# Performance work log

Hardware: AMD Instinct MI355X
Metric: run time of the kernel (lower is better)

Reference implementation:

```python
import jax, jax.numpy as jnp
import numpy as np

B_, L_, D_, E_, N_, DR_, DC_ = 2, 2048, 1024, 2048, 16, 64, 4

def setup_inputs() -> dict:
    key = jax.random.key(0)
    ks = jax.random.split(key, 12)
    s = lambda fan: 1.0 / np.sqrt(fan)
    inp = {}
    inp['resid'] = jax.random.normal(ks[0], (B_, L_, D_), jnp.float32)
    inp['norm_w'] = jnp.ones((D_,), jnp.float32)
    inp['skip_w'] = jax.random.normal(ks[1], (E_, D_), jnp.float32) * s(D_)
    inp['in_w'] = jax.random.normal(ks[2], (E_, D_), jnp.float32) * s(D_)
    inp['conv_w'] = jax.random.normal(ks[3], (E_, DC_), jnp.float32) * s(DC_)
    inp['conv_b'] = jax.random.normal(ks[4], (E_,), jnp.float32) * 0.1
    inp['wd1'] = jax.random.normal(ks[5], (DR_, E_), jnp.float32) * s(E_)
    inp['wd2'] = jax.random.uniform(ks[6], (E_, DR_), jnp.float32, -1.0, 1.0) * (DR_ ** -0.5)
    # dt bias init: inverse softplus of dt in [dt_min, dt_max]
    dt = jnp.exp(jax.random.uniform(ks[7], (E_,), jnp.float32) * (np.log(0.1) - np.log(0.001)) + np.log(0.001))
    dt = jnp.clip(dt, 1e-4, None)
    inp['wd2_b'] = dt + jnp.log(-jnp.expm1(-dt))
    inp['wB'] = jax.random.normal(ks[8], (N_, E_), jnp.float32) * s(E_)
    inp['wC'] = jax.random.normal(ks[9], (N_, E_), jnp.float32) * s(E_)
    inp['A_log'] = jnp.log(jnp.broadcast_to(jnp.arange(1, N_ + 1, dtype=jnp.float32), (E_, N_)))
    inp['W_D'] = jnp.ones((E_,), jnp.float32)
    inp['out_w'] = jax.random.normal(ks[10], (D_, E_), jnp.float32) * s(E_)
    return inp


def reference(resid, norm_w, skip_w, in_w, conv_w, conv_b, wd1, wd2, wd2_b, wB, wC, A_log, W_D, out_w):
    eps = 1e-5
    # RMSNorm
    xn = resid * jax.lax.rsqrt(jnp.mean(resid * resid, axis=-1, keepdims=True) + eps) * norm_w
    skip = jnp.einsum('bld,ed->ble', xn, skip_w)          # [B,L,E]
    x = jnp.einsum('bld,ed->ble', xn, in_w)               # [B,L,E]
    # causal depthwise conv1d (padding d_conv-1, keep first L outputs)
    Dc = conv_w.shape[1]
    L = x.shape[1]
    xp = jnp.pad(x, ((0, 0), (Dc - 1, 0), (0, 0)))
    xc = conv_b + sum(xp[:, k:k + L, :] * conv_w[:, k] for k in range(Dc))
    x = jax.nn.silu(xc)                                   # ssm input [B,L,E]
    # input-dependent delta, B, C
    delta = jax.nn.softplus(jnp.einsum('blr,er->ble', jnp.einsum('ble,re->blr', x, wd1), wd2) + wd2_b)
    Bm = jnp.einsum('ble,ne->bln', x, wB)                 # [B,L,N]
    Cm = jnp.einsum('ble,ne->bln', x, wC)                 # [B,L,N]
    A = -jnp.exp(A_log)                                   # [E,N]
    # selective scan over L
    def step(h, inp):
        xt, dt, bt, ct = inp                              # [B,E],[B,E],[B,N],[B,N]
        h = jnp.exp(dt[:, :, None] * A) * h + (dt * xt)[:, :, None] * bt[:, None, :]
        y = jnp.einsum('ben,bn->be', h, ct)
        return h, y
    h0 = jnp.zeros((x.shape[0], A.shape[0], A.shape[1]), x.dtype)
    xs = (jnp.swapaxes(x, 0, 1), jnp.swapaxes(delta, 0, 1),
          jnp.swapaxes(Bm, 0, 1), jnp.swapaxes(Cm, 0, 1))
    _, ys = jax.lax.scan(step, h0, xs)                    # ys: [L,B,E]
    y = jnp.swapaxes(ys, 0, 1) + W_D * x                  # skip connection D*x
    y = y * jax.nn.silu(skip)                             # gate
    out = jnp.einsum('ble,de->bld', y, out_w)
    return resid + out
```

## Files before the change

### kernel.cpp

```cpp
#include <hip/hip_runtime.h>
#include <hip/hip_bf16.h>

#define B_ 2
#define L_ 2048
#define D_ 1024
#define E_ 2048
#define N_ 16
#define DR_ 64
#define DC_ 4
#define M_ (B_*L_)
#define SSEG 16
#define LSEG (L_/SSEG)
#define KS_ 8
#define CH 32
#define LOG2E 1.4426950408889634f

typedef __attribute__((ext_vector_type(8))) short bf16x8;
typedef __attribute__((ext_vector_type(4))) float f32x4;

__device__ __forceinline__ ushort f2bf(float x){
    union { float f; unsigned u; } v; v.f = x;
    unsigned r = v.u + 0x7FFFu + ((v.u >> 16) & 1u);
    return (ushort)(r >> 16);
}
__device__ __forceinline__ float bf2f(ushort u){
    union { unsigned u; float f; } v; v.u = ((unsigned)u) << 16;
    return v.f;
}
__device__ __forceinline__ float fexp2(float x){
    float r;
    asm("v_exp_f32 %0, %1" : "=v"(r) : "v"(x));
    return r;
}
__device__ __forceinline__ float fast_silu(float x){
    return x * __builtin_amdgcn_rcpf(1.f + __expf(-x));
}
__device__ __forceinline__ float softplus_f(float z){
    return (z > 20.f) ? z : __logf(1.f + __expf(z));
}

#define DPP_F(x, CTRL) __int_as_float(__builtin_amdgcn_update_dpp(0, __float_as_int(x), (CTRL), 0xf, 0xf, true))

__device__ __forceinline__ void gld16(const void* g, void* l){
    __builtin_amdgcn_global_load_lds(
        (const __attribute__((address_space(1))) unsigned int*)g,
        (__attribute__((address_space(3))) unsigned int*)l,
        16, 0, 0);
}

#define PR0 (E_*D_/4)
#define PR1 (2*PR0)
#define PR2 (3*PR0)
#define PR3 (PR2 + E_*DR_/4)
#define PR4 (PR3 + DR_*E_/4)
#define PR5 (PR4 + N_*E_/4)
#define PR6 (PR5 + N_*E_/4)
#define PR7 (PR6 + 32*E_/4)
#define PR8 (PR7 + 4*E_/4)
__global__ __launch_bounds__(256) void prep_k(const float* __restrict__ in_w,
                                              const float* __restrict__ skip_w,
                                              const float* __restrict__ out_w,
                                              const float* __restrict__ wd2,
                                              const float* __restrict__ wd1,
                                              const float* __restrict__ wB,
                                              const float* __restrict__ wC,
                                              const float* __restrict__ conv_w,
                                              ushort* __restrict__ wis,
                                              ushort* __restrict__ wo,
                                              ushort* __restrict__ wd2b,
                                              ushort* __restrict__ W96,
                                              float* __restrict__ cwT){
    int i = blockIdx.x * 256 + threadIdx.x;
    const float* src; ushort* dst; int off;
    if (i < PR0)      { src = in_w;   dst = wis;                       off = i; }
    else if (i < PR1) { src = skip_w; dst = wis + (size_t)E_*D_;       off = i - PR0; }
    else if (i < PR2) { src = out_w;  dst = wo;                        off = i - PR1; }
    else if (i < PR3) { src = wd2;    dst = wd2b;                      off = i - PR2; }
    else if (i < PR4) { src = wd1;    dst = W96;                       off = i - PR3; }
    else if (i < PR5) { src = wB;     dst = W96 + (size_t)64*E_;       off = i - PR4; }
    else if (i < PR6) { src = wC;     dst = W96 + (size_t)80*E_;       off = i - PR5; }
    else if (i < PR7) {
        ushort4 z = {0,0,0,0};
        ((ushort4*)(W96 + (size_t)96*E_))[i - PR6] = z;
        return;
    } else if (i < PR8) {
        int u = i - PR7;
        int k = u >> 9;
        int g = u & 511;
        float4 o;
        o.x = conv_w[(g*4 + 0)*4 + k];
        o.y = conv_w[(g*4 + 1)*4 + k];
        o.z = conv_w[(g*4 + 2)*4 + k];
        o.w = conv_w[(g*4 + 3)*4 + k];
        ((float4*)(cwT + (size_t)k * E_))[g] = o;
        return;
    } else return;
    float4 v = ((const float4*)src)[off];
    ushort4 o;
    o.x = f2bf(v.x); o.y = f2bf(v.y); o.z = f2bf(v.z); o.w = f2bf(v.w);
    ((ushort4*)dst)[off] = o;
}

__global__ __launch_bounds__(256) void rmsnorm_k(const float* __restrict__ resid,
                                                 const float* __restrict__ norm_w,
                                                 ushort* __restrict__ xn){
    int row = blockIdx.x;
    const float4* r = (const float4*)(resid + (size_t)row * D_);
    float4 v = r[threadIdx.x];
    float ss = v.x*v.x + v.y*v.y + v.z*v.z + v.w*v.w;
    for (int m = 32; m; m >>= 1) ss += __shfl_xor(ss, m);
    __shared__ float sred[4];
    if ((threadIdx.x & 63) == 0) sred[threadIdx.x >> 6] = ss;
    __syncthreads();
    float tot = sred[0] + sred[1] + sred[2] + sred[3];
    float scale = rsqrtf(tot / (float)D_ + 1e-5f);
    const float4* wv = (const float4*)norm_w;
    float4 w = wv[threadIdx.x];
    ushort4 o;
    o.x = f2bf(v.x * scale * w.x);
    o.y = f2bf(v.y * scale * w.y);
    o.z = f2bf(v.z * scale * w.z);
    o.w = f2bf(v.w * scale * w.w);
    ((ushort4*)(xn + (size_t)row * D_))[threadIdx.x] = o;
}

#define BM 128
#define BN 128
#define BK 64

__global__ __launch_bounds__(256)
void gemm_dual_k(const ushort* __restrict__ A, const ushort* __restrict__ Bm,
                 ushort* __restrict__ P1, ushort* __restrict__ P2){
    __shared__ __align__(16) ushort As[BM * BK];
    __shared__ __align__(16) ushort Bs[BN * BK];
    const int wid9 = (blockIdx.x & 7) * 128 + (blockIdx.x >> 3);
    const int col0 = (wid9 & 31) * BN;
    const int row0 = (wid9 >> 5) * BM;
    const int tid = threadIdx.x;
    const int lane = tid & 63;
    const int wid = tid >> 6;
    const int wm = wid >> 1, wn = wid & 1;
    f32x4 acc[4][4] = {};
    const int l8 = lane >> 3;
    const int cs = ((lane & 7) ^ (l8 & 7)) * 8;

    for (int k0 = 0; k0 < D_; k0 += BK){
        #pragma unroll
        for (int i = 0; i < 4; ++i){
            const int R0 = wid * 32 + i * 8;
            gld16(A + (size_t)(row0 + R0 + l8) * D_ + k0 + cs, As + R0 * BK);
            gld16(Bm + (size_t)(col0 + R0 + l8) * D_ + k0 + cs, Bs + R0 * BK);
        }
        __syncthreads();
        #pragma unroll
        for (int kk = 0; kk < 2; ++kk){
            bf16x8 af[4], bfr[4];
            const int krow = lane & 15;
            const int kcol = ((kk * 4 + (lane >> 4)) ^ (krow & 7)) * 8;
            #pragma unroll
            for (int mi = 0; mi < 4; ++mi)
                af[mi] = *(const bf16x8*)(As + (wm*64 + mi*16 + krow) * BK + kcol);
            #pragma unroll
            for (int ni = 0; ni < 4; ++ni)
                bfr[ni] = *(const bf16x8*)(Bs + (wn*64 + ni*16 + krow) * BK + kcol);
            #pragma unroll
            for (int mi = 0; mi < 4; ++mi)
                #pragma unroll
                for (int ni = 0; ni < 4; ++ni)
                    acc[mi][ni] = __builtin_amdgcn_mfma_f32_16x16x32_bf16(af[mi], bfr[ni], acc[mi][ni], 0, 0, 0);
        }
        __syncthreads();
    }
    ushort* base = (col0 < E_) ? P1 : P2;
    const int cb = (col0 < E_) ? col0 : col0 - E_;
    #pragma unroll
    for (int mi = 0; mi < 4; ++mi)
        #pragma unroll
        for (int ni = 0; ni < 4; ++ni)
            #pragma unroll
            for (int j = 0; j < 4; ++j){
                int r = row0 + wm*64 + mi*16 + (lane >> 4) * 4 + j;
                int c = cb + wn*64 + ni*16 + (lane & 15);
                base[(size_t)r * E_ + c] = f2bf(acc[mi][ni][j]);
            }
}

#define OBM 64
__global__ __launch_bounds__(256)
void gemm_out_k(const ushort* __restrict__ A, const ushort* __restrict__ Bm,
                float* __restrict__ Cp, const float* __restrict__ aux){
    __shared__ __align__(16) ushort As[OBM * BK];
    __shared__ __align__(16) ushort Bs[BN * BK];
    const int wid9 = (blockIdx.x & 7) * 64 + (blockIdx.x >> 3);
    const int col0 = (wid9 & 7) * BN;
    const int row0 = (wid9 >> 3) * OBM;
    const int tid = threadIdx.x;
    const int lane = tid & 63;
    const int wid = tid >> 6;
    const int wm = wid >> 1, wn = wid & 1;
    f32x4 acc[2][4] = {};
    const int l8 = lane >> 3;
    const int cs = ((lane & 7) ^ (l8 & 7)) * 8;

    for (int k0 = 0; k0 < E_; k0 += BK){
        #pragma unroll
        for (int i = 0; i < 2; ++i){
            const int R0 = wid * 16 + i * 8;
            gld16(A + (size_t)(row0 + R0 + l8) * E_ + k0 + cs, As + R0 * BK);
        }
        #pragma unroll
        for (int i = 0; i < 4; ++i){
            const int R0 = wid * 32 + i * 8;
            gld16(Bm + (size_t)(col0 + R0 + l8) * E_ + k0 + cs, Bs + R0 * BK);
        }
        __syncthreads();
        #pragma unroll
        for (int kk = 0; kk < 2; ++kk){
            bf16x8 af[2], bfr[4];
            const int krow = lane & 15;
            const int kcol = ((kk * 4 + (lane >> 4)) ^ (krow & 7)) * 8;
            #pragma unroll
            for (int mi = 0; mi < 2; ++mi)
                af[mi] = *(const bf16x8*)(As + (wm*32 + mi*16 + krow) * BK + kcol);
            #pragma unroll
            for (int ni = 0; ni < 4; ++ni)
                bfr[ni] = *(const bf16x8*)(Bs + (wn*64 + ni*16 + krow) * BK + kcol);
            #pragma unroll
            for (int mi = 0; mi < 2; ++mi)
                #pragma unroll
                for (int ni = 0; ni < 4; ++ni)
                    acc[mi][ni] = __builtin_amdgcn_mfma_f32_16x16x32_bf16(af[mi], bfr[ni], acc[mi][ni], 0, 0, 0);
        }
        __syncthreads();
    }
    #pragma unroll
    for (int mi = 0; mi < 2; ++mi)
        #pragma unroll
        for (int ni = 0; ni < 4; ++ni)
            #pragma unroll
            for (int j = 0; j < 4; ++j){
                int r = row0 + wm*32 + mi*16 + (lane >> 4) * 4 + j;
                int c = col0 + wn*64 + ni*16 + (lane & 15);
                size_t idx = (size_t)r * D_ + c;
                Cp[idx] = acc[mi][ni][j] + aux[idx];
            }
}

#define CBM 64
__global__ __launch_bounds__(256)
void gemm_c96_sk(const ushort* __restrict__ A, const ushort* __restrict__ Bm,
                 float* __restrict__ part){
    __shared__ __align__(16) ushort As[CBM * BK];
    __shared__ __align__(16) ushort Bs[128 * BK];
    const int ks = blockIdx.x;
    const int row0 = blockIdx.y * CBM;
    const int tid = threadIdx.x;
    const int lane = tid & 63;
    const int wid = tid >> 6;
    const int wm = wid >> 1, wn = wid & 1;
    f32x4 acc[2][4] = {};
    const int l8 = lane >> 3;
    const int cs = ((lane & 7) ^ (l8 & 7)) * 8;

    for (int k0 = ks * (E_ / KS_); k0 < (ks + 1) * (E_ / KS_); k0 += BK){
        #pragma unroll
        for (int i = 0; i < 2; ++i){
            const int R0 = wid * 16 + i * 8;
            gld16(A + (size_t)(row0 + R0 + l8) * E_ + k0 + cs, As + R0 * BK);
        }
        #pragma unroll
        for (int i = 0; i < 4; ++i){
            const int R0 = wid * 32 + i * 8;
            gld16(Bm + (size_t)(R0 + l8) * E_ + k0 + cs, Bs + R0 * BK);
        }
        __syncthreads();
        #pragma unroll
        for (int kk = 0; kk < 2; ++kk){
            bf16x8 af[2], bfr[4];
            const int krow = lane & 15;
            const int kcol = ((kk * 4 + (lane >> 4)) ^ (krow & 7)) * 8;
            #pragma unroll
            for (int mi = 0; mi < 2; ++mi)
                af[mi] = *(const bf16x8*)(As + (wm*32 + mi*16 + krow) * BK + kcol);
            #pragma unroll
            for (int ni = 0; ni < 4; ++ni)
                bfr[ni] = *(const bf16x8*)(Bs + (wn*64 + ni*16 + krow) * BK + kcol);
            #pragma unroll
            for (int mi = 0; mi < 2; ++mi)
                #pragma unroll
                for (int ni = 0; ni < 4; ++ni)
                    acc[mi][ni] = __builtin_amdgcn_mfma_f32_16x16x32_bf16(af[mi], bfr[ni], acc[mi][ni], 0, 0, 0);
        }
        __syncthreads();
    }
    float* dst = part + (size_t)ks * M_ * 128;
    #pragma unroll
    for (int mi = 0; mi < 2; ++mi)
        #pragma unroll
        for (int ni = 0; ni < 4; ++ni)
            #pragma unroll
            for (int j = 0; j < 4; ++j){
                int r = row0 + wm*32 + mi*16 + (lane >> 4) * 4 + j;
                int c = wn*64 + ni*16 + (lane & 15);
                dst[(size_t)r * 128 + c] = acc[mi][ni][j];
            }
}

__global__ __launch_bounds__(256) void c96_reduce_k(const float* __restrict__ part,
                                                    ushort* __restrict__ C96){
    int i4 = blockIdx.x * 256 + threadIdx.x;
    float4 a = *(const float4*)(part + (size_t)i4 * 4);
    #pragma unroll
    for (int k = 1; k < KS_; ++k){
        float4 b = *(const float4*)(part + (size_t)k * M_ * 128 + (size_t)i4 * 4);
        a.x += b.x; a.y += b.y; a.z += b.z; a.w += b.w;
    }
    ushort4 o;
    o.x = f2bf(a.x); o.y = f2bf(a.y); o.z = f2bf(a.z); o.w = f2bf(a.w);
    *(ushort4*)(C96 + (size_t)i4 * 4) = o;
}

__global__ __launch_bounds__(256) void conv_silu_k(const ushort* __restrict__ xpre,
                                                   const float* __restrict__ cwT,
                                                   const float* __restrict__ conv_b,
                                                   ushort* __restrict__ xb){
    int i4 = blockIdx.x * 256 + threadIdx.x;
    if (i4 >= M_ * E_ / 4) return;
    int idx = i4 * 4;
    int e = idx & (E_ - 1);
    int bl = idx >> 11;
    int t = bl & (L_ - 1);
    float4 b4 = *(const float4*)(conv_b + e);
    float a0 = b4.x, a1 = b4.y, a2 = b4.z, a3 = b4.w;
    #pragma unroll
    for (int k = 0; k < 4; ++k){
        int dt = 3 - k;
        if (t >= dt){
            ushort4 xv = *(const ushort4*)(xpre + idx - dt * E_);
            float4 wv = *(const float4*)(cwT + (size_t)k * E_ + e);
            a0 += bf2f(xv.x) * wv.x;
            a1 += bf2f(xv.y) * wv.y;
            a2 += bf2f(xv.z) * wv.z;
            a3 += bf2f(xv.w) * wv.w;
        }
    }
    ushort4 sb;
    sb.x = f2bf(fast_silu(a0));
    sb.y = f2bf(fast_silu(a1));
    sb.z = f2bf(fast_silu(a2));
    sb.w = f2bf(fast_silu(a3));
    *(ushort4*)(xb + idx) = sb;
}

#define SF2 36
#define SYD 20

__device__ __forceinline__ void seg_swz(int& b, int& s, int& e0){
    int lin = blockIdx.x + 128 * (blockIdx.y + 16 * blockIdx.z);
    int swz = (lin & 7) * 512 + (lin >> 3);
    e0 = (swz & 127) * 16;
    s  = (swz >> 7) & 15;
    b  = swz >> 11;
}

__global__ __launch_bounds__(256, 8) void seg1_k(const ushort* __restrict__ xb,
                                              const ushort* __restrict__ C96,
                                              const ushort* __restrict__ wd2b,
                                              const float* __restrict__ wd2_bias,
                                              const float* __restrict__ A_log,
                                              float* __restrict__ F,
                                              float* __restrict__ segdt){
    int b, s, e0; seg_swz(b, s, e0);
    const int tid = threadIdx.x;
    const int lane = tid & 63, wid = tid >> 6;
    const int n = tid & 15, ei = tid >> 4;
    const int e = e0 + ei;
    const float Aen2 = -__expf(A_log[e * N_ + n]) * LOG2E;
    float h = 0.f;
    __shared__ __align__(16) ushort sxr[CH][72];
    __shared__ __align__(16) ushort swd2[16][72];
    __shared__ __align__(16) ushort sxu[16][40];
    __shared__ float sd[16][SF2], sdx[16][SF2], sB[16][SF2];
    __shared__ float ssdt[2][16];
    const int tq = tid >> 3, qc = tid & 7;

    if (tid < 128){
        int r = tid >> 3, cc = (tid & 7) * 8;
        *(uint4*)&swd2[r][cc] = *(const uint4*)(wd2b + (size_t)(e0 + r) * DR_ + cc);
    }
    const float bias = wd2_bias[e0 + (lane & 15)];
    float psdt = 0.f;

    for (int c = 0; c < LSEG / CH; ++c){
        int t0 = s * LSEG + c * CH;
        size_t row = (size_t)(b * L_ + t0 + tq);
        *(uint4*)&sxr[tq][qc * 8] = *(const uint4*)(C96 + row * 128 + qc * 8);
        ushort2 rB = *(const ushort2*)(C96 + row * 128 + 64 + qc * 2);
        ushort2 xu = *(const ushort2*)(xb + row * E_ + e0 + qc * 2);
        sB[qc*2+0][tq] = bf2f(rB.x); sB[qc*2+1][tq] = bf2f(rB.y);
        sxu[qc*2+0][tq] = xu.x; sxu[qc*2+1][tq] = xu.y;
        __syncthreads();
        if (wid < 2){
            f32x4 dacc = {};
            #pragma unroll
            for (int kk = 0; kk < 2; ++kk){
                bf16x8 af = *(const bf16x8*)&sxr[wid*16 + (lane & 15)][kk*32 + (lane >> 4)*8];
                bf16x8 bf = *(const bf16x8*)&swd2[lane & 15][kk*32 + (lane >> 4)*8];
                dacc = __builtin_amdgcn_mfma_f32_16x16x32_bf16(af, bf, dacc, 0, 0, 0);
            }
            const int crow = lane & 15;
            const int ttc = wid*16 + (lane >> 4)*4;
            float4 dv;
            dv.x = softplus_f(dacc[0] + bias);
            dv.y = softplus_f(dacc[1] + bias);
            dv.z = softplus_f(dacc[2] + bias);
            dv.w = softplus_f(dacc[3] + bias);
            *(float4*)&sd[crow][ttc] = dv;
            psdt += dv.x + dv.y + dv.z + dv.w;
            ushort4 xu4 = *(const ushort4*)&sxu[crow][ttc];
            float4 dxv;
            dxv.x = dv.x * bf2f(xu4.x); dxv.y = dv.y * bf2f(xu4.y);
            dxv.z = dv.z * bf2f(xu4.z); dxv.w = dv.w * bf2f(xu4.w);
            *(float4*)&sdx[crow][ttc] = dxv;
        }
        __syncthreads();
        #pragma unroll
        for (int t = 0; t < CH; t += 4){
            float4 d4  = *(const float4*)&sd[ei][t];
            float4 dx4 = *(const float4*)&sdx[ei][t];
            float4 b4  = *(const float4*)&sB[n][t];
            h = fexp2(d4.x*Aen2)*h + dx4.x*b4.x;
            h = fexp2(d4.y*Aen2)*h + dx4.y*b4.y;
            h = fexp2(d4.z*Aen2)*h + dx4.z*b4.z;
            h = fexp2(d4.w*Aen2)*h + dx4.w*b4.w;
        }
        __syncthreads();
    }
    if (wid < 2){
        psdt += __shfl_xor(psdt, 16);
        psdt += __shfl_xor(psdt, 32);
        if (lane < 16) ssdt[wid][lane] = psdt;
    }
    size_t base = ((size_t)(b * SSEG + s) * E_ + e) * N_ + n;
    F[base] = h;
    __syncthreads();
    if (tid < 16)
        segdt[(size_t)(b * SSEG + s) * E_ + e0 + tid] = ssdt[0][tid] + ssdt[1][tid];
}

__global__ __launch_bounds__(256) void carry_k(const float* __restrict__ F,
                                               const float* __restrict__ segdt,
                                               const float* __restrict__ A_log,
                                               float* __restrict__ carr){
    int idx = blockIdx.x * 256 + threadIdx.x;
    int n = idx & 15;
    int e = (idx >> 4) & (E_ - 1);
    int b = idx >> 15;
    const float Aen2 = -__expf(A_log[e * N_ + n]) * LOG2E;
    float c = 0.f;
    #pragma unroll
    for (int s = 0; s < SSEG; ++s){
        size_t base = ((size_t)(b * SSEG + s) * E_ + e) * N_ + n;
        carr[base] = c;
        float P = fexp2(Aen2 * segdt[(size_t)(b * SSEG + s) * E_ + e]);
        c = P * c + F[base];
    }
}

__global__ __launch_bounds__(256, 8) void seg2_k(const ushort* __restrict__ xb,
                                              const ushort* __restrict__ C96,
                                              const ushort* __restrict__ wd2b,
                                              const float* __restrict__ wd2_bias,
                                              const float* __restrict__ A_log,
                                              const float* __restrict__ carr,
                                              const ushort* __restrict__ skipb,
                                              const float* __restrict__ W_D,
                                              ushort* __restrict__ y2){
    int b, s, e0; seg_swz(b, s, e0);
    const int tid = threadIdx.x;
    const int lane = tid & 63, wid = tid >> 6;
    const int n = tid & 15, ei = tid >> 4;
    const int e = e0 + ei;
    const float Aen2 = -__expf(A_log[e * N_ + n]) * LOG2E;
    float h = carr[((size_t)(b * SSEG + s) * E_ + e) * N_ + n];
    __shared__ __align__(16) ushort sxr[CH][72];
    __shared__ __align__(16) ushort swd2[16][72];
    __shared__ __align__(16) ushort sxu[16][40];
    __shared__ float sd[16][SF2], sdx[16][SF2], sB[16][SF2], sC[16][SF2];
    __shared__ float sy[CH][SYD];
    const int tq = tid >> 3, qc = tid & 7;

    if (tid < 128){
        int r = tid >> 3, cc = (tid & 7) * 8;
        *(uint4*)&swd2[r][cc] = *(const uint4*)(wd2b + (size_t)(e0 + r) * DR_ + cc);
    }
    const float bias = wd2_bias[e0 + (lane & 15)];
    const float wv0 = W_D[e0 + qc * 2], wv1 = W_D[e0 + qc * 2 + 1];

    for (int c = 0; c < LSEG / CH; ++c){
        int t0 = s * LSEG + c * CH;
        size_t row = (size_t)(b * L_ + t0 + tq);
        *(uint4*)&sxr[tq][qc * 8] = *(const uint4*)(C96 + row * 128 + qc * 8);
        ushort2 rB = *(const ushort2*)(C96 + row * 128 + 64 + qc * 2);
        ushort2 rC = *(const ushort2*)(C96 + row * 128 + 80 + qc * 2);
        ushort2 xu = *(const ushort2*)(xb + row * E_ + e0 + qc * 2);
        ushort2 sv_pre = *(const ushort2*)(skipb + row * E_ + e0 + qc * 2);
        sB[qc*2+0][tq] = bf2f(rB.x); sB[qc*2+1][tq] = bf2f(rB.y);
        sC[qc*2+0][tq] = bf2f(rC.x); sC[qc*2+1][tq] = bf2f(rC.y);
        sxu[qc*2+0][tq] = xu.x; sxu[qc*2+1][tq] = xu.y;
        __syncthreads();
        if (wid < 2){
            f32x4 dacc = {};
            #pragma unroll
            for (int kk = 0; kk < 2; ++kk){
                bf16x8 af = *(const bf16x8*)&sxr[wid*16 + (lane & 15)][kk*32 + (lane >> 4)*8];
                bf16x8 bf = *(const bf16x8*)&swd2[lane & 15][kk*32 + (lane >> 4)*8];
                dacc = __builtin_amdgcn_mfma_f32_16x16x32_bf16(af, bf, dacc, 0, 0, 0);
            }
            const int crow = lane & 15;
            const int ttc = wid*16 + (lane >> 4)*4;
            float4 dv;
            dv.x = softplus_f(dacc[0] + bias);
            dv.y = softplus_f(dacc[1] + bias);
            dv.z = softplus_f(dacc[2] + bias);
            dv.w = softplus_f(dacc[3] + bias);
            *(float4*)&sd[crow][ttc] = dv;
            ushort4 xu4 = *(const ushort4*)&sxu[crow][ttc];
            float4 dxv;
            dxv.x = dv.x * bf2f(xu4.x); dxv.y = dv.y * bf2f(xu4.y);
            dxv.z = dv.z * bf2f(xu4.z); dxv.w = dv.w * bf2f(xu4.w);
            *(float4*)&sdx[crow][ttc] = dxv;
        }
        __syncthreads();
        #pragma unroll
        for (int t = 0; t < CH; t += 4){
            float4 d4  = *(const float4*)&sd[ei][t];
            float4 dx4 = *(const float4*)&sdx[ei][t];
            float4 b4  = *(const float4*)&sB[n][t];
            float4 c4  = *(const float4*)&sC[n][t];
            float y0, y1, y2v, y3;
            h = fexp2(d4.x*Aen2)*h + dx4.x*b4.x;  y0 = h * c4.x;
            h = fexp2(d4.y*Aen2)*h + dx4.y*b4.y;  y1 = h * c4.y;
            h = fexp2(d4.z*Aen2)*h + dx4.z*b4.z;  y2v = h * c4.z;
            h = fexp2(d4.w*Aen2)*h + dx4.w*b4.w;  y3 = h * c4.w;
            float s01 = (n & 1) ? y0 : y1;
            float r01 = DPP_F(s01, 0xB1);
            float s23 = (n & 1) ? y2v : y3;
            float r23 = DPP_F(s23, 0xB1);
            float va, vb;
            if (n & 1){ va = y1 + r01; vb = y3 + r23; }
            else      { va = y0 + r01; vb = y2v + r23; }
            float s2 = (n & 2) ? va : vb;
            float r2 = DPP_F(s2, 0x4E);
            float v = ((n & 2) ? vb : va) + r2;
            v += DPP_F(v, 0x124);
            v += DPP_F(v, 0x128);
            if (n < 4) sy[t + n][ei] = v;
        }
        __syncthreads();
        {
            size_t orow = (size_t)(b * L_ + t0 + tq);
            float yv0 = sy[tq][qc*2], yv1 = sy[tq][qc*2+1];
            float xs0 = bf2f(sxu[qc*2+0][tq]), xs1 = bf2f(sxu[qc*2+1][tq]);
            float sk0 = bf2f(sv_pre.x), sk1 = bf2f(sv_pre.y);
            ushort2 o;
            o.x = f2bf((yv0 + wv0 * xs0) * fast_silu(sk0));
            o.y = f2bf((yv1 + wv1 * xs1) * fast_silu(sk1));
            *(ushort2*)(y2 + orow * E_ + e0 + qc * 2) = o;
        }
        __syncthreads();
    }
}

extern "C" void kernel_launch(void* const* d_in, const int* in_sizes, int n_in,
                              void* d_out, int out_size, void* d_ws, size_t ws_size,
                              hipStream_t stream){
    const float* resid  = (const float*)d_in[0];
    const float* norm_w = (const float*)d_in[1];
    const float* skip_w = (const float*)d_in[2];
    const float* in_w   = (const float*)d_in[3];
    const float* conv_w = (const float*)d_in[4];
    const float* conv_b = (const float*)d_in[5];
    const float* wd1    = (const float*)d_in[6];
    const float* wd2    = (const float*)d_in[7];
    const float* wd2_b  = (const float*)d_in[8];
    const float* wB     = (const float*)d_in[9];
    const float* wC     = (const float*)d_in[10];
    const float* A_log  = (const float*)d_in[11];
    const float* W_D    = (const float*)d_in[12];
    const float* out_w  = (const float*)d_in[13];
    float* out = (float*)d_out;

    char* ws = (char*)d_ws;
    size_t off = 0;
    auto alloc = [&](size_t bytes) -> char* {
        char* p = ws + off;
        off += (bytes + 255) & ~(size_t)255;
        return p;
    };
    char* alias_base = ws;
    ushort* wis_b   = (ushort*)alloc((size_t)2 * E_ * D_ * 2);
    ushort* xn_b    = (ushort*)alloc((size_t)M_ * D_ * 2);
    ushort* xpre_b  = (ushort*)alloc((size_t)M_ * E_ * 2);
    float*  part_buf= (float*)alias_base;
    ushort* wo_b    = (ushort*)alloc((size_t)D_ * E_ * 2);
    ushort* wd2_bf  = (ushort*)alloc((size_t)E_ * DR_ * 2);
    ushort* W96_b   = (ushort*)alloc((size_t)128 * E_ * 2);
    float*  cwT_b   = (float*)alloc((size_t)4 * E_ * 4);
    ushort* skip_b  = (ushort*)alloc((size_t)M_ * E_ * 2);
    ushort* xb_b    = (ushort*)alloc((size_t)M_ * E_ * 2);
    ushort* C96_b   = (ushort*)alloc((size_t)M_ * 128 * 2);
    float*  scr     = (float*)alloc((size_t)9 * 1024 * 1024);
    ushort* y2_b    = (ushort*)alloc((size_t)M_ * E_ * 2);
    float* F_buf    = scr;
    float* carr_buf = scr + (size_t)B_ * SSEG * E_ * N_;
    float* segdt_buf= scr + (size_t)2 * B_ * SSEG * E_ * N_;
    (void)ws_size; (void)in_sizes; (void)n_in; (void)out_size;

    const int thr = 256;

    prep_k<<<(PR8 + 255)/256, thr, 0, stream>>>(in_w, skip_w, out_w, wd2, wd1, wB, wC, conv_w,
                                                wis_b, wo_b, wd2_bf, W96_b, cwT_b);

    rmsnorm_k<<<M_, thr, 0, stream>>>(resid, norm_w, xn_b);

    gemm_dual_k<<<1024, thr, 0, stream>>>(xn_b, wis_b, xpre_b, skip_b);

    conv_silu_k<<<(M_*E_/4 + 255)/256, thr, 0, stream>>>(xpre_b, cwT_b, conv_b, xb_b);

    gemm_c96_sk<<<dim3(KS_, M_/CBM), thr, 0, stream>>>(xb_b, W96_b, part_buf);
    c96_reduce_k<<<(M_*128/4)/256, thr, 0, stream>>>(part_buf, C96_b);

    seg1_k<<<dim3(E_/16, SSEG, B_), thr, 0, stream>>>(xb_b, C96_b, wd2_bf, wd2_b, A_log, F_buf, segdt_buf);
    carry_k<<<(B_*E_*N_)/256, thr, 0, stream>>>(F_buf, segdt_buf, A_log, carr_buf);
    seg2_k<<<dim3(E_/16, SSEG, B_), thr, 0, stream>>>(xb_b, C96_b, wd2_bf, wd2_b, A_log, carr_buf,
                                                      skip_b, W_D, y2_b);

    gemm_out_k<<<512, thr, 0, stream>>>(y2_b, wo_b, out, resid);
}
```

Baseline: 201.2 us.

## Double-buffer LDS tiles in input and output GEMMs; remap dual GEMM blocks per XCD

Both bf16 MFMA GEMMs now keep two LDS buffers and issue the global-to-LDS loads for the next K tile before computing on the current one, so memory latency can overlap with MFMA work. The dual GEMM also changes its block-to-tile mapping so each XCD gets a contiguous 16x8 patch of output tiles, which is meant to improve L2 reuse of the A and B panels. The cost is double the LDS per block, which may lower occupancy. It also depends on gld16 completion being ordered by the single __syncthreads per iteration.

```diff
diff --git a/kernel.cpp b/kernel.cpp
--- a/kernel.cpp
+++ b/kernel.cpp
@@ -131,11 +131,12 @@
 __global__ __launch_bounds__(256)
 void gemm_dual_k(const ushort* __restrict__ A, const ushort* __restrict__ Bm,
                  ushort* __restrict__ P1, ushort* __restrict__ P2){
-    __shared__ __align__(16) ushort As[BM * BK];
-    __shared__ __align__(16) ushort Bs[BN * BK];
-    const int wid9 = (blockIdx.x & 7) * 128 + (blockIdx.x >> 3);
-    const int col0 = (wid9 & 31) * BN;
-    const int row0 = (wid9 >> 5) * BM;
+    __shared__ __align__(16) ushort As[2][BM * BK];
+    __shared__ __align__(16) ushort Bs[2][BN * BK];
+    const int xcd = blockIdx.x & 7;
+    const int idx = blockIdx.x >> 3;
+    const int row0 = (((xcd >> 2) << 4) + (idx >> 3)) * BM;
+    const int col0 = (((xcd & 3) << 3) + (idx & 7)) * BN;
     const int tid = threadIdx.x;
     const int lane = tid & 63;
     const int wid = tid >> 6;
@@ -144,14 +145,25 @@
     const int l8 = lane >> 3;
     const int cs = ((lane & 7) ^ (l8 & 7)) * 8;
 
-    for (int k0 = 0; k0 < D_; k0 += BK){
-        #pragma unroll
-        for (int i = 0; i < 4; ++i){
-            const int R0 = wid * 32 + i * 8;
-            gld16(A + (size_t)(row0 + R0 + l8) * D_ + k0 + cs, As + R0 * BK);
-            gld16(Bm + (size_t)(col0 + R0 + l8) * D_ + k0 + cs, Bs + R0 * BK);
-        }
-        __syncthreads();
+    const int NK = D_ / BK;
+    #pragma unroll
+    for (int i = 0; i < 4; ++i){
+        const int R0 = wid * 32 + i * 8;
+        gld16(A + (size_t)(row0 + R0 + l8) * D_ + cs, &As[0][R0 * BK]);
+        gld16(Bm + (size_t)(col0 + R0 + l8) * D_ + cs, &Bs[0][R0 * BK]);
+    }
+    __syncthreads();
+    int cur = 0;
+    for (int ki = 0; ki < NK; ++ki){
+        if (ki + 1 < NK){
+            const int k0 = (ki + 1) * BK;
+            #pragma unroll
+            for (int i = 0; i < 4; ++i){
+                const int R0 = wid * 32 + i * 8;
+                gld16(A + (size_t)(row0 + R0 + l8) * D_ + k0 + cs, &As[cur^1][R0 * BK]);
+                gld16(Bm + (size_t)(col0 + R0 + l8) * D_ + k0 + cs, &Bs[cur^1][R0 * BK]);
+            }
+        }
         #pragma unroll
         for (int kk = 0; kk < 2; ++kk){
             bf16x8 af[4], bfr[4];
@@ -159,10 +171,10 @@
             const int kcol = ((kk * 4 + (lane >> 4)) ^ (krow & 7)) * 8;
             #pragma unroll
             for (int mi = 0; mi < 4; ++mi)
-                af[mi] = *(const bf16x8*)(As + (wm*64 + mi*16 + krow) * BK + kcol);
+                af[mi] = *(const bf16x8*)(&As[cur][(wm*64 + mi*16 + krow) * BK + kcol]);
             #pragma unroll
             for (int ni = 0; ni < 4; ++ni)
-                bfr[ni] = *(const bf16x8*)(Bs + (wn*64 + ni*16 + krow) * BK + kcol);
+                bfr[ni] = *(const bf16x8*)(&Bs[cur][(wn*64 + ni*16 + krow) * BK + kcol]);
             #pragma unroll
             for (int mi = 0; mi < 4; ++mi)
                 #pragma unroll
@@ -170,6 +182,7 @@
                     acc[mi][ni] = __builtin_amdgcn_mfma_f32_16x16x32_bf16(af[mi], bfr[ni], acc[mi][ni], 0, 0, 0);
         }
         __syncthreads();
+        cur ^= 1;
     }
     ushort* base = (col0 < E_) ? P1 : P2;
     const int cb = (col0 < E_) ? col0 : col0 - E_;
@@ -189,8 +202,8 @@
 __global__ __launch_bounds__(256)
 void gemm_out_k(const ushort* __restrict__ A, const ushort* __restrict__ Bm,
                 float* __restrict__ Cp, const float* __restrict__ aux){
-    __shared__ __align__(16) ushort As[OBM * BK];
-    __shared__ __align__(16) ushort Bs[BN * BK];
+    __shared__ __align__(16) ushort As[2][OBM * BK];
+    __shared__ __align__(16) ushort Bs[2][BN * BK];
     const int wid9 = (blockIdx.x & 7) * 64 + (blockIdx.x >> 3);
     const int col0 = (wid9 & 7) * BN;
     const int row0 = (wid9 >> 3) * OBM;
@@ -202,18 +215,33 @@
     const int l8 = lane >> 3;
     const int cs = ((lane & 7) ^ (l8 & 7)) * 8;
 
-    for (int k0 = 0; k0 < E_; k0 += BK){
-        #pragma unroll
-        for (int i = 0; i < 2; ++i){
-            const int R0 = wid * 16 + i * 8;
-            gld16(A + (size_t)(row0 + R0 + l8) * E_ + k0 + cs, As + R0 * BK);
-        }
-        #pragma unroll
-        for (int i = 0; i < 4; ++i){
-            const int R0 = wid * 32 + i * 8;
-            gld16(Bm + (size_t)(col0 + R0 + l8) * E_ + k0 + cs, Bs + R0 * BK);
-        }
-        __syncthreads();
+    const int NK = E_ / BK;
+    #pragma unroll
+    for (int i = 0; i < 2; ++i){
+        const int R0 = wid * 16 + i * 8;
+        gld16(A + (size_t)(row0 + R0 + l8) * E_ + cs, &As[0][R0 * BK]);
+    }
+    #pragma unroll
+    for (int i = 0; i < 4; ++i){
+        const int R0 = wid * 32 + i * 8;
+        gld16(Bm + (size_t)(col0 + R0 + l8) * E_ + cs, &Bs[0][R0 * BK]);
+    }
+    __syncthreads();
+    int cur = 0;
+    for (int ki = 0; ki < NK; ++ki){
+        if (ki + 1 < NK){
+            const int k0 = (ki + 1) * BK;
+            #pragma unroll
+            for (int i = 0; i < 2; ++i){
+                const int R0 = wid * 16 + i * 8;
+                gld16(A + (size_t)(row0 + R0 + l8) * E_ + k0 + cs, &As[cur^1][R0 * BK]);
+            }
+            #pragma unroll
+            for (int i = 0; i < 4; ++i){
+                const int R0 = wid * 32 + i * 8;
+                gld16(Bm + (size_t)(col0 + R0 + l8) * E_ + k0 + cs, &Bs[cur^1][R0 * BK]);
+            }
+        }
         #pragma unroll
         for (int kk = 0; kk < 2; ++kk){
             bf16x8 af[2], bfr[4];
@@ -221,10 +249,10 @@
             const int kcol = ((kk * 4 + (lane >> 4)) ^ (krow & 7)) * 8;
             #pragma unroll
             for (int mi = 0; mi < 2; ++mi)
-                af[mi] = *(const bf16x8*)(As + (wm*32 + mi*16 + krow) * BK + kcol);
+                af[mi] = *(const bf16x8*)(&As[cur][(wm*32 + mi*16 + krow) * BK + kcol]);
             #pragma unroll
             for (int ni = 0; ni < 4; ++ni)
-                bfr[ni] = *(const bf16x8*)(Bs + (wn*64 + ni*16 + krow) * BK + kcol);
+                bfr[ni] = *(const bf16x8*)(&Bs[cur][(wn*64 + ni*16 + krow) * BK + kcol]);
             #pragma unroll
             for (int mi = 0; mi < 2; ++mi)
                 #pragma unroll
@@ -232,6 +260,7 @@
                     acc[mi][ni] = __builtin_amdgcn_mfma_f32_16x16x32_bf16(af[mi], bfr[ni], acc[mi][ni], 0, 0, 0);
         }
         __syncthreads();
+        cur ^= 1;
     }
     #pragma unroll
     for (int mi = 0; mi < 2; ++mi)
```

Measured after the change: 199.7 us. No clear change (-0.8%).
